# Performance work log

Hardware: AMD Instinct MI355X
Metric: run time of the kernel (lower is better)

Reference implementation:

```python
import jax, jax.numpy as jnp
import numpy as np

B, S, L = 256, 512, 128


def setup_inputs() -> dict:
    key = jax.random.key(0)
    k0, k1, k2, k3, k4, k5 = jax.random.split(key, 6)
    features = jax.random.normal(k0, (B, S, L), dtype=jnp.float32)
    attention_mask = jnp.ones((B, S), dtype=jnp.int32)  # all positions valid
    labels = jax.random.randint(k1, (B, S), 0, L)
    confidence = jax.random.uniform(k2, (B,), dtype=jnp.float32)
    start_transitions = jax.random.uniform(k3, (L,), minval=-0.1, maxval=0.1)
    end_transitions = jax.random.uniform(k4, (L,), minval=-0.1, maxval=0.1)
    transitions = jax.random.uniform(k5, (L, L), minval=-0.1, maxval=0.1)
    return {
        "features": features,
        "start_transitions": start_transitions,
        "end_transitions": end_transitions,
        "transitions": transitions,
        "confidence": confidence,
        "attention_mask": attention_mask,
        "labels": labels,
    }


def _crf_loss(features, start_transitions, end_transitions, transitions,
              confidence, attention_mask, labels):
    # time-major, matching torch.swapaxes(features, 0, 1)
    feats = jnp.swapaxes(features, 0, 1)                    # [S,B,L]
    mask = jnp.swapaxes(attention_mask, 0, 1).astype(bool)  # [S,B]
    labs = jnp.swapaxes(jnp.where(labels == -100, 0, labels), 0, 1)  # [S,B]
    bs = feats.shape[1]
    barange = jnp.arange(bs)

    # ---- log numerator (gold path score), fully vectorized over time ----
    emit = jnp.take_along_axis(feats, labs[:, :, None], axis=2)[..., 0]  # [S,B]
    trans_scores = transitions[labs[:-1], labs[1:]]                      # [S-1,B]
    maskf = mask[1:].astype(feats.dtype)
    log_num = (start_transitions[labs[0]] + emit[0]
               + jnp.sum((trans_scores + emit[1:]) * maskf, axis=0))
    seq_lens = mask.sum(axis=0) - 1                                      # [B]
    last_tags = labs[seq_lens, barange]
    log_num = log_num + end_transitions[last_tags]

    # ---- log denominator (partition function) via sequential scan ----
    def step(alpha, xs):
        feat_t, mask_t = xs  # [B,L], [B]
        nxt = jax.nn.logsumexp(
            alpha[:, :, None] + transitions[None, :, :] + feat_t[:, None, :],
            axis=1)
        return jnp.where(mask_t[:, None], nxt, alpha), None

    alpha0 = start_transitions + feats[0]                    # [B,L]
    alpha, _ = jax.lax.scan(step, alpha0, (feats[1:], mask[1:]))
    log_den = jax.nn.logsumexp(alpha + end_transitions, axis=1)  # [B]

    loss = (log_den - log_num) * confidence
    return jnp.mean(loss)


def reference(features, start_transitions, end_transitions, transitions,
              confidence, attention_mask, labels):
    return _crf_loss(features, start_transitions, end_transitions, transitions,
                     confidence, attention_mask, labels)
```

## Files before the change

kernel.cpp:

```cpp
#include <hip/hip_runtime.h>
#include <hip/hip_bf16.h>
#include <math.h>

#define NB 256
#define SS 512
#define LL 128

typedef short bf16x8 __attribute__((ext_vector_type(8)));
typedef float f32x4 __attribute__((ext_vector_type(4)));

template <int P>
__device__ __forceinline__ float swzf(float x) {
    return __int_as_float(__builtin_amdgcn_ds_swizzle(__float_as_int(x), P));
}
__device__ __forceinline__ short f2bf(float f) {
    __hip_bfloat16 h = __float2bfloat16(f);
    short s;
    __builtin_memcpy(&s, &h, 2);
    return s;
}
__device__ __forceinline__ float bf2f(short s) {
    return __int_as_float(((int)(unsigned short)s) << 16);
}

__global__ __launch_bounds__(256, 2) void crf_chain_kernel(
    const float* __restrict__ feats,
    const float* __restrict__ start_t,
    const float* __restrict__ end_t,
    const float* __restrict__ trans,
    const int* __restrict__ mask,
    const int* __restrict__ labels,
    float* __restrict__ ws)
{
    const int bid = blockIdx.x;
    const int b = bid & 255;
    const int isB = bid >> 8;
    const int tid = threadIdx.x;
    const int w = tid >> 6;
    const int L = tid & 63;
    const int l15 = L & 15;
    const int g = L >> 4;
    const int myNt = 2 * w + (g & 1);
    const int p_own = 16 * myNt + l15;

    __shared__ __align__(16) short img[2][LL];
    __shared__ __align__(16) short fS[128 * LL];
    __shared__ int lmask[SS];
    __shared__ float nred[4];
    __shared__ int cred[4];

    float* av = ws;
    float* bv = ws + NB * LL;
    float* eFa = ws + 2 * NB * LL;
    float* eBa = eFa + NB;
    float* lognum = eBa + NB;

    const float* fb = feats + (size_t)b * SS * LL;

    bf16x8 Bf[4][2];
#pragma unroll
    for (int kt = 0; kt < 4; ++kt) {
#pragma unroll
        for (int jj = 0; jj < 2; ++jj) {
            int n = 16 * (2 * w + jj) + l15;
            bf16x8 fr;
#pragma unroll
            for (int j2 = 0; j2 < 8; ++j2) {
                int k = 32 * kt + 8 * g + j2;
                float v = isB ? trans[n * LL + k] : trans[k * LL + n];
                fr[j2] = f2bf(__expf(v));
            }
            Bf[kt][jj] = fr;
        }
    }

    lmask[tid] = mask[b * SS + tid];
    lmask[tid + 256] = mask[b * SS + tid + 256];

    float x;
    if (isB) x = __expf(end_t[p_own]);
    else     x = __expf(start_t[p_own] + fb[p_own]);
    int eacc = 0;

    for (int r = 0; r < 256; ++r) {
        if ((r & 127) == 0) {
            if (r) __syncthreads();
            const int s = r >> 7;
#pragma unroll
            for (int q = 0; q < 16; ++q) {
                int v = tid + 256 * q;
                int slot = v >> 5;
                int pos4 = v & 31;
                int t = isB ? (511 - (128 * s + slot)) : (1 + 128 * s + slot);
                const float4 f4 = *(const float4*)(fb + (size_t)t * LL + 4 * pos4);
                short4 o;
                o.x = f2bf(f4.x); o.y = f2bf(f4.y); o.z = f2bf(f4.z); o.w = f2bf(f4.w);
                *((short4*)&fS[slot * LL + 4 * pos4]) = o;
            }
            __syncthreads();
        }

        const int t = isB ? (511 - r) : (r + 1);
        float ft = bf2f(fS[(r & 127) * LL + p_own]);
        int mt = lmask[t];
        if (r == 255 && !isB) mt = 0;

        float pub = isB ? __expf(ft) * x : x;
        if (g < 2) img[r & 1][p_own] = f2bf(pub);
        __syncthreads();

        const bf16x8* ip = (const bf16x8*)(&img[r & 1][0]);
        bf16x8 a0 = ip[g], a1 = ip[4 + g], a2 = ip[8 + g], a3 = ip[12 + g];
        f32x4 c0 = {0.f, 0.f, 0.f, 0.f}, c1 = {0.f, 0.f, 0.f, 0.f};
        c0 = __builtin_amdgcn_mfma_f32_16x16x32_bf16(a0, Bf[0][0], c0, 0, 0, 0);
        c1 = __builtin_amdgcn_mfma_f32_16x16x32_bf16(a0, Bf[0][1], c1, 0, 0, 0);
        c0 = __builtin_amdgcn_mfma_f32_16x16x32_bf16(a1, Bf[1][0], c0, 0, 0, 0);
        c1 = __builtin_amdgcn_mfma_f32_16x16x32_bf16(a1, Bf[1][1], c1, 0, 0, 0);
        c0 = __builtin_amdgcn_mfma_f32_16x16x32_bf16(a2, Bf[2][0], c0, 0, 0, 0);
        c1 = __builtin_amdgcn_mfma_f32_16x16x32_bf16(a2, Bf[2][1], c1, 0, 0, 0);
        c0 = __builtin_amdgcn_mfma_f32_16x16x32_bf16(a3, Bf[3][0], c0, 0, 0, 0);
        c1 = __builtin_amdgcn_mfma_f32_16x16x32_bf16(a3, Bf[3][1], c1, 0, 0, 0);

        float cpre = (g & 1) ? c1[0] : c0[0];
        float cand = isB ? cpre : __expf(ft) * cpre;
        x = mt ? cand : x;

        if ((r & 7) == 7) {
            float s = 0.f;
#pragma unroll
            for (int i = 0; i < 8; ++i)
                s += bf2f(a0[i]) + bf2f(a1[i]) + bf2f(a2[i]) + bf2f(a3[i]);
            s += swzf<0x401F>(s);
            s += __shfl_xor(s, 32);
            int ex;
            frexpf(s, &ex);
            x = ldexpf(x, -ex);
            eacc += ex;
        }
    }

    if (g < 2) { (isB ? bv : av)[b * LL + p_own] = x; }
    if (tid == 0) { (isB ? eBa : eFa)[b] = (float)eacc; }

    if (isB) {
        const int* lb = labels + b * SS;
        const int* mb = mask + b * SS;
        float term = 0.f;
        int cnt = 0;
#pragma unroll
        for (int rr = 0; rr < 2; ++rr) {
            int tt = tid + rr * 256;
            int l = lb[tt];
            if ((unsigned)l >= LL) l = 0;
            int m = mb[tt];
            cnt += (m != 0);
            if (tt == 0) {
                term += start_t[l] + fb[l];
            } else if (m) {
                int lp = lb[tt - 1];
                if ((unsigned)lp >= LL) lp = 0;
                term += trans[lp * LL + l] + fb[(size_t)tt * LL + l];
            }
        }
#pragma unroll
        for (int o = 1; o < 64; o <<= 1) {
            term += __shfl_xor(term, o);
            cnt += __shfl_xor(cnt, o);
        }
        if (L == 0) { nred[w] = term; cred[w] = cnt; }
        __syncthreads();
        if (tid == 0) {
            float tot = nred[0] + nred[1] + nred[2] + nred[3];
            int c = cred[0] + cred[1] + cred[2] + cred[3];
            int sl = c - 1;
            sl = sl < 0 ? 0 : (sl >= SS ? SS - 1 : sl);
            int lt = lb[sl];
            if ((unsigned)lt >= LL) lt = 0;
            lognum[b] = tot + end_t[lt];
        }
    }
}

__global__ __launch_bounds__(256) void crf_final_kernel(
    const float* __restrict__ ws, const float* __restrict__ conf,
    float* __restrict__ out)
{
    const int tid = threadIdx.x;
    const float* av = ws;
    const float* bv = ws + NB * LL;
    const float* eFa = ws + 2 * NB * LL;
    const float* eBa = eFa + NB;
    const float* ln = eBa + NB;

    const float4* a4 = (const float4*)(av + tid * LL);
    const float4* b4 = (const float4*)(bv + tid * LL);
    float dot = 0.f;
#pragma unroll 8
    for (int k = 0; k < 32; ++k) {
        float4 a = a4[k], bb = b4[k];
        dot += a.x * bb.x + a.y * bb.y + a.z * bb.z + a.w * bb.w;
    }
    float logZ = logf(dot) + 0.69314718055994531f * (eFa[tid] + eBa[tid]);
    float loss = (logZ - ln[tid]) * conf[tid] * (1.0f / NB);

#pragma unroll
    for (int o = 1; o < 64; o <<= 1) loss += __shfl_xor(loss, o);
    __shared__ float red[4];
    if ((tid & 63) == 0) red[tid >> 6] = loss;
    __syncthreads();
    if (tid == 0) out[0] = red[0] + red[1] + red[2] + red[3];
}

extern "C" void kernel_launch(void* const* d_in, const int* in_sizes, int n_in,
                              void* d_out, int out_size, void* d_ws, size_t ws_size,
                              hipStream_t stream) {
    const float* feats  = (const float*)d_in[0];
    const float* startt = (const float*)d_in[1];
    const float* endt   = (const float*)d_in[2];
    const float* trans  = (const float*)d_in[3];
    const float* conf   = (const float*)d_in[4];
    const int*   mask   = (const int*)d_in[5];
    const int*   labels = (const int*)d_in[6];
    float* out = (float*)d_out;
    float* ws = (float*)d_ws;

    hipLaunchKernelGGL(crf_chain_kernel, dim3(2 * NB), dim3(256), 0, stream,
                       feats, startt, endt, trans, mask, labels, ws);
    hipLaunchKernelGGL(crf_final_kernel, dim3(1), dim3(256), 0, stream,
                       ws, conf, out);
}
```

Measured before the change: 210.0 us.

## Run each CRF direction in a single wave, removing per-step block barriers

Each sequence now gets one 128-thread block, with one wavefront for the forward recursion and one for the backward. Each wave holds all 8 column tiles of exp(transitions) in registers and does the full 128x128 MFMA product per step itself. This removes the per-step __syncthreads and the shared-memory feature staging, and feature rows are register-prefetched two steps ahead from global memory. The final reduction is fused in through an atomicAdd after a memset. The cost is 8x more MFMA work per wave, much higher register pressure (32 B fragments), and atomic float ordering nondeterminism.

```diff
diff --git a/kernel.cpp b/kernel.cpp
--- a/kernel.cpp
+++ b/kernel.cpp
@@ -19,147 +19,162 @@
     __builtin_memcpy(&s, &h, 2);
     return s;
 }
-__device__ __forceinline__ float bf2f(short s) {
-    return __int_as_float(((int)(unsigned short)s) << 16);
-}
-
-__global__ __launch_bounds__(256, 2) void crf_chain_kernel(
+
+__global__ __launch_bounds__(128, 1) void crf_kernel(
     const float* __restrict__ feats,
     const float* __restrict__ start_t,
     const float* __restrict__ end_t,
     const float* __restrict__ trans,
+    const float* __restrict__ conf,
     const int* __restrict__ mask,
     const int* __restrict__ labels,
-    float* __restrict__ ws)
+    float* __restrict__ out)
 {
-    const int bid = blockIdx.x;
-    const int b = bid & 255;
-    const int isB = bid >> 8;
+    const int b = blockIdx.x;
     const int tid = threadIdx.x;
-    const int w = tid >> 6;
-    const int L = tid & 63;
-    const int l15 = L & 15;
-    const int g = L >> 4;
-    const int myNt = 2 * w + (g & 1);
-    const int p_own = 16 * myNt + l15;
+    const int isB = tid >> 6;
+    const int l = tid & 63;
+    const int l15 = l & 15;
+    const int g = l >> 4;
 
     __shared__ __align__(16) short img[2][LL];
-    __shared__ __align__(16) short fS[128 * LL];
     __shared__ int lmask[SS];
-    __shared__ float nred[4];
-    __shared__ int cred[4];
-
-    float* av = ws;
-    float* bv = ws + NB * LL;
-    float* eFa = ws + 2 * NB * LL;
-    float* eBa = eFa + NB;
-    float* lognum = eBa + NB;
+    __shared__ float sv[2][LL];
+    __shared__ float sc[4];
+
+#pragma unroll
+    for (int q = 0; q < 4; ++q)
+        lmask[tid + 128 * q] = mask[b * SS + tid + 128 * q];
+    __syncthreads();
 
     const float* fb = feats + (size_t)b * SS * LL;
 
-    bf16x8 Bf[4][2];
+    bf16x8 Bf[4][8];
 #pragma unroll
     for (int kt = 0; kt < 4; ++kt) {
 #pragma unroll
-        for (int jj = 0; jj < 2; ++jj) {
-            int n = 16 * (2 * w + jj) + l15;
+        for (int nt = 0; nt < 8; ++nt) {
+            const int n = 16 * nt + l15;
             bf16x8 fr;
 #pragma unroll
-            for (int j2 = 0; j2 < 8; ++j2) {
-                int k = 32 * kt + 8 * g + j2;
-                float v = isB ? trans[n * LL + k] : trans[k * LL + n];
-                fr[j2] = f2bf(__expf(v));
-            }
-            Bf[kt][jj] = fr;
-        }
-    }
-
-    lmask[tid] = mask[b * SS + tid];
-    lmask[tid + 256] = mask[b * SS + tid + 256];
-
-    float x;
-    if (isB) x = __expf(end_t[p_own]);
-    else     x = __expf(start_t[p_own] + fb[p_own]);
+            for (int j = 0; j < 8; ++j) {
+                const int k = 32 * kt + 8 * g + j;
+                const float v = isB ? trans[n * LL + k] : trans[k * LL + n];
+                fr[j] = f2bf(__expf(v));
+            }
+            Bf[kt][nt] = fr;
+        }
+    }
+
+    float x[8];
+#pragma unroll
+    for (int nt = 0; nt < 8; ++nt) {
+        const int n = 16 * nt + l15;
+        x[nt] = isB ? __expf(end_t[n]) : __expf(start_t[n] + fb[n]);
+    }
     int eacc = 0;
 
-    for (int r = 0; r < 256; ++r) {
-        if ((r & 127) == 0) {
-            if (r) __syncthreads();
-            const int s = r >> 7;
-#pragma unroll
-            for (int q = 0; q < 16; ++q) {
-                int v = tid + 256 * q;
-                int slot = v >> 5;
-                int pos4 = v & 31;
-                int t = isB ? (511 - (128 * s + slot)) : (1 + 128 * s + slot);
-                const float4 f4 = *(const float4*)(fb + (size_t)t * LL + 4 * pos4);
-                short4 o;
-                o.x = f2bf(f4.x); o.y = f2bf(f4.y); o.z = f2bf(f4.z); o.w = f2bf(f4.w);
-                *((short4*)&fS[slot * LL + 4 * pos4]) = o;
-            }
-            __syncthreads();
-        }
-
-        const int t = isB ? (511 - r) : (r + 1);
-        float ft = bf2f(fS[(r & 127) * LL + p_own]);
-        int mt = lmask[t];
-        if (r == 255 && !isB) mt = 0;
-
-        float pub = isB ? __expf(ft) * x : x;
-        if (g < 2) img[r & 1][p_own] = f2bf(pub);
-        __syncthreads();
-
-        const bf16x8* ip = (const bf16x8*)(&img[r & 1][0]);
-        bf16x8 a0 = ip[g], a1 = ip[4 + g], a2 = ip[8 + g], a3 = ip[12 + g];
-        f32x4 c0 = {0.f, 0.f, 0.f, 0.f}, c1 = {0.f, 0.f, 0.f, 0.f};
-        c0 = __builtin_amdgcn_mfma_f32_16x16x32_bf16(a0, Bf[0][0], c0, 0, 0, 0);
-        c1 = __builtin_amdgcn_mfma_f32_16x16x32_bf16(a0, Bf[0][1], c1, 0, 0, 0);
-        c0 = __builtin_amdgcn_mfma_f32_16x16x32_bf16(a1, Bf[1][0], c0, 0, 0, 0);
-        c1 = __builtin_amdgcn_mfma_f32_16x16x32_bf16(a1, Bf[1][1], c1, 0, 0, 0);
-        c0 = __builtin_amdgcn_mfma_f32_16x16x32_bf16(a2, Bf[2][0], c0, 0, 0, 0);
-        c1 = __builtin_amdgcn_mfma_f32_16x16x32_bf16(a2, Bf[2][1], c1, 0, 0, 0);
-        c0 = __builtin_amdgcn_mfma_f32_16x16x32_bf16(a3, Bf[3][0], c0, 0, 0, 0);
-        c1 = __builtin_amdgcn_mfma_f32_16x16x32_bf16(a3, Bf[3][1], c1, 0, 0, 0);
-
-        float cpre = (g & 1) ? c1[0] : c0[0];
-        float cand = isB ? cpre : __expf(ft) * cpre;
-        x = mt ? cand : x;
-
-        if ((r & 7) == 7) {
-            float s = 0.f;
-#pragma unroll
-            for (int i = 0; i < 8; ++i)
-                s += bf2f(a0[i]) + bf2f(a1[i]) + bf2f(a2[i]) + bf2f(a3[i]);
-            s += swzf<0x401F>(s);
-            s += __shfl_xor(s, 32);
-            int ex;
-            frexpf(s, &ex);
-            x = ldexpf(x, -ex);
-            eacc += ex;
-        }
-    }
-
-    if (g < 2) { (isB ? bv : av)[b * LL + p_own] = x; }
-    if (tid == 0) { (isB ? eBa : eFa)[b] = (float)eacc; }
+    auto tof = [&](int r) { return isB ? (511 - r) : (r + 1); };
+
+    float fp[2][8];
+    int mp[2];
+#pragma unroll
+    for (int h = 0; h < 2; ++h) {
+        const float* rowp = fb + (size_t)tof(h) * LL;
+#pragma unroll
+        for (int nt = 0; nt < 8; ++nt) fp[h][nt] = rowp[16 * nt + l15];
+        mp[h] = lmask[tof(h)];
+    }
+
+    short* const myimg = img[isB];
+
+    for (int rp = 0; rp < 128; ++rp) {
+#pragma unroll
+        for (int h = 0; h < 2; ++h) {
+            const int r = 2 * rp + h;
+            float ft[8];
+#pragma unroll
+            for (int nt = 0; nt < 8; ++nt) ft[nt] = fp[h][nt];
+            int mt = mp[h];
+            if (r == 255 && !isB) mt = 0;
+
+            if (rp < 127) {
+                const float* rowp = fb + (size_t)tof(r + 2) * LL;
+#pragma unroll
+                for (int nt = 0; nt < 8; ++nt)
+                    fp[h][nt] = rowp[16 * nt + l15];
+                mp[h] = lmask[tof(r + 2)];
+            }
+
+#pragma unroll
+            for (int gg = 0; gg < 2; ++gg) {
+                const int nt = 2 * g + gg;
+                const float pub = isB ? __expf(ft[nt]) * x[nt] : x[nt];
+                myimg[16 * nt + l15] = f2bf(pub);
+            }
+
+            bf16x8 a[4];
+#pragma unroll
+            for (int kt = 0; kt < 4; ++kt)
+                __builtin_memcpy(&a[kt], &myimg[32 * kt + 8 * g], 16);
+
+            f32x4 c[8];
+#pragma unroll
+            for (int nt = 0; nt < 8; ++nt) {
+                f32x4 cc = {0.f, 0.f, 0.f, 0.f};
+                cc = __builtin_amdgcn_mfma_f32_16x16x32_bf16(a[0], Bf[0][nt], cc, 0, 0, 0);
+                cc = __builtin_amdgcn_mfma_f32_16x16x32_bf16(a[1], Bf[1][nt], cc, 0, 0, 0);
+                cc = __builtin_amdgcn_mfma_f32_16x16x32_bf16(a[2], Bf[2][nt], cc, 0, 0, 0);
+                cc = __builtin_amdgcn_mfma_f32_16x16x32_bf16(a[3], Bf[3][nt], cc, 0, 0, 0);
+                c[nt] = cc;
+            }
+
+#pragma unroll
+            for (int nt = 0; nt < 8; ++nt) {
+                const float cand = isB ? c[nt][0] : __expf(ft[nt]) * c[nt][0];
+                x[nt] = mt ? cand : x[nt];
+            }
+
+            if ((r & 7) == 7) {
+                float s = 0.f;
+#pragma unroll
+                for (int nt = 0; nt < 8; ++nt) s += x[nt];
+                s += swzf<0x041F>(s);
+                s += swzf<0x081F>(s);
+                s += swzf<0x101F>(s);
+                s += swzf<0x201F>(s);
+                int ex;
+                frexpf(s, &ex);
+#pragma unroll
+                for (int nt = 0; nt < 8; ++nt) x[nt] = ldexpf(x[nt], -ex);
+                eacc += ex;
+            }
+        }
+    }
+
+    if (g == 0) {
+#pragma unroll
+        for (int nt = 0; nt < 8; ++nt) sv[isB][16 * nt + l15] = x[nt];
+    }
+    if (l == 0) sc[isB] = (float)eacc;
 
     if (isB) {
         const int* lb = labels + b * SS;
-        const int* mb = mask + b * SS;
         float term = 0.f;
         int cnt = 0;
 #pragma unroll
-        for (int rr = 0; rr < 2; ++rr) {
-            int tt = tid + rr * 256;
-            int l = lb[tt];
-            if ((unsigned)l >= LL) l = 0;
-            int m = mb[tt];
+        for (int rr = 0; rr < 8; ++rr) {
+            const int tt = l + 64 * rr;
+            int lc = lb[tt];
+            if ((unsigned)lc >= LL) lc = 0;
+            const int m = lmask[tt];
             cnt += (m != 0);
             if (tt == 0) {
-                term += start_t[l] + fb[l];
+                term += start_t[lc] + fb[lc];
             } else if (m) {
                 int lp = lb[tt - 1];
                 if ((unsigned)lp >= LL) lp = 0;
-                term += trans[lp * LL + l] + fb[(size_t)tt * LL + l];
+                term += trans[lp * LL + lc] + fb[(size_t)tt * LL + lc];
             }
         }
 #pragma unroll
@@ -167,48 +182,28 @@
             term += __shfl_xor(term, o);
             cnt += __shfl_xor(cnt, o);
         }
-        if (L == 0) { nred[w] = term; cred[w] = cnt; }
-        __syncthreads();
-        if (tid == 0) {
-            float tot = nred[0] + nred[1] + nred[2] + nred[3];
-            int c = cred[0] + cred[1] + cred[2] + cred[3];
-            int sl = c - 1;
+        if (l == 0) {
+            int sl = cnt - 1;
             sl = sl < 0 ? 0 : (sl >= SS ? SS - 1 : sl);
             int lt = lb[sl];
             if ((unsigned)lt >= LL) lt = 0;
-            lognum[b] = tot + end_t[lt];
-        }
-    }
-}
-
-__global__ __launch_bounds__(256) void crf_final_kernel(
-    const float* __restrict__ ws, const float* __restrict__ conf,
-    float* __restrict__ out)
-{
-    const int tid = threadIdx.x;
-    const float* av = ws;
-    const float* bv = ws + NB * LL;
-    const float* eFa = ws + 2 * NB * LL;
-    const float* eBa = eFa + NB;
-    const float* ln = eBa + NB;
-
-    const float4* a4 = (const float4*)(av + tid * LL);
-    const float4* b4 = (const float4*)(bv + tid * LL);
-    float dot = 0.f;
-#pragma unroll 8
-    for (int k = 0; k < 32; ++k) {
-        float4 a = a4[k], bb = b4[k];
-        dot += a.x * bb.x + a.y * bb.y + a.z * bb.z + a.w * bb.w;
-    }
-    float logZ = logf(dot) + 0.69314718055994531f * (eFa[tid] + eBa[tid]);
-    float loss = (logZ - ln[tid]) * conf[tid] * (1.0f / NB);
-
-#pragma unroll
-    for (int o = 1; o < 64; o <<= 1) loss += __shfl_xor(loss, o);
-    __shared__ float red[4];
-    if ((tid & 63) == 0) red[tid >> 6] = loss;
+            sc[2] = term + end_t[lt];
+        }
+    }
+
     __syncthreads();
-    if (tid == 0) out[0] = red[0] + red[1] + red[2] + red[3];
+
+    if (tid < 64) {
+        float p = sv[0][l] * sv[1][l] + sv[0][l + 64] * sv[1][l + 64];
+#pragma unroll
+        for (int o = 1; o < 64; o <<= 1) p += __shfl_xor(p, o);
+        if (l == 0) {
+            const float logZ =
+                logf(p) + 0.69314718055994531f * (sc[0] + sc[1]);
+            const float loss = (logZ - sc[2]) * conf[b] * (1.0f / NB);
+            atomicAdd(out, loss);
+        }
+    }
 }
 
 extern "C" void kernel_launch(void* const* d_in, const int* in_sizes, int n_in,
@@ -222,10 +217,8 @@
     const int*   mask   = (const int*)d_in[5];
     const int*   labels = (const int*)d_in[6];
     float* out = (float*)d_out;
-    float* ws = (float*)d_ws;
-
-    hipLaunchKernelGGL(crf_chain_kernel, dim3(2 * NB), dim3(256), 0, stream,
-                       feats, startt, endt, trans, mask, labels, ws);
-    hipLaunchKernelGGL(crf_final_kernel, dim3(1), dim3(256), 0, stream,
-                       ws, conf, out);
-}
+
+    hipMemsetAsync(d_out, 0, sizeof(float), stream);
+    hipLaunchKernelGGL(crf_kernel, dim3(NB), dim3(128), 0, stream,
+                       feats, startt, endt, trans, conf, mask, labels, out);
+}
```

New measurement: 264.2 us. 1.26x slower.
